# Optimization experiments

Measured on AMD Instinct MI355X. Metric: run time of the kernel, lower is better.

Reference implementation:

```python
import jax, jax.numpy as jnp
import numpy as np

B, N, M, C1, C2, H = 16, 4096, 1024, 256, 512, 256
SE_C = max(1, int(H / 24.0))  # 10
BN_EPS = 1e-5

def _bn(x, g, b):
    # training-mode BatchNorm over (B, n) per channel; x: [B, C, n]
    mean = jnp.mean(x, axis=(0, 2), keepdims=True)
    var = jnp.mean((x - mean) ** 2, axis=(0, 2), keepdims=True)  # biased var (torch)
    return (x - mean) * jax.lax.rsqrt(var + BN_EPS) * g[None, :, None] + b[None, :, None]

def _swish(x):
    return x * jax.nn.sigmoid(x)

def setup_inputs() -> dict:
    key = jax.random.key(0)
    ks = jax.random.split(key, 12)
    d = {
        "unknown": jax.random.normal(ks[0], (B, N, 3), jnp.float32),
        "known": jax.random.normal(ks[1], (B, M, 3), jnp.float32),
        "unknow_feats": jax.random.normal(ks[2], (B, C1, N), jnp.float32),
        "known_feats": jax.random.normal(ks[3], (B, C2, M), jnp.float32),
        # conv1 (C1+C2 -> H), no bias (bn)
        "W1": jax.random.normal(ks[4], (H, C1 + C2), jnp.float32) * (1.0 / np.sqrt(C1 + C2)),
        "g1": jnp.ones((H,), jnp.float32),
        "b1": jnp.zeros((H,), jnp.float32),
        # SE block (1x1 convs with bias, no pooling in this impl)
        "se_rw": jax.random.normal(ks[5], (SE_C, H), jnp.float32) * (1.0 / np.sqrt(H)),
        "se_rb": jnp.zeros((SE_C,), jnp.float32),
        "se_ew": jax.random.normal(ks[6], (H, SE_C), jnp.float32) * (1.0 / np.sqrt(SE_C)),
        "se_eb": jnp.zeros((H,), jnp.float32),
        # conv2 (H -> H), no bias
        "W2": jax.random.normal(ks[7], (H, H), jnp.float32) * (1.0 / np.sqrt(H)),
        "g2": jnp.ones((H,), jnp.float32),
        "b2": jnp.zeros((H,), jnp.float32),
    }
    return d

def reference(unknown, known, unknow_feats, known_feats,
              W1, g1, b1, se_rw, se_rb, se_ew, se_eb, W2, g2, b2):
    # three_nn: squared distances of each unknown point to all known points
    d2 = jnp.sum((unknown[:, :, None, :] - known[:, None, :, :]) ** 2, axis=-1)  # [B,N,M]
    neg_d, idx = jax.lax.top_k(-d2, 3)  # 3 smallest
    dist = -neg_d                                       # [B,N,3]
    dist_recip = 1.0 / (dist + 1e-8)
    weight = dist_recip / jnp.sum(dist_recip, axis=2, keepdims=True)  # [B,N,3]
    # three_interpolate: gather known_feats at idx, inverse-distance weighted sum
    gathered = jnp.take_along_axis(known_feats[:, :, None, :], idx[:, None, :, :], axis=3)  # [B,C2,N,3]
    interp = jnp.sum(gathered * weight[:, None, :, :], axis=-1)  # [B,C2,N]
    x = jnp.concatenate([interp, unknow_feats], axis=1)  # [B,C1+C2,N]
    # conv1 (1x1) + BN + SE
    h = jnp.einsum('oc,bcn->bon', W1, x)
    h = _bn(h, g1, b1)
    s = jnp.einsum('oc,bcn->bon', se_rw, h) + se_rb[None, :, None]
    s = _swish(s)
    s = jnp.einsum('oc,bcn->bon', se_ew, s) + se_eb[None, :, None]
    h = jax.nn.sigmoid(s) * h
    # conv2 (1x1) + BN + ReLU
    h = jnp.einsum('oc,bcn->bon', W2, h)
    h = _bn(h, g2, b2)
    return jax.nn.relu(h)  # [B, H, N]
```

## Files before the change

kernel.cpp:

```cpp
#include <hip/hip_runtime.h>
#include <math.h>

#define B_ 16
#define N_ 4096
#define M_ 1024
#define C1_ 256
#define C2_ 512
#define H_ 256
#define SEC_ 10
#define PARTS_ 128
#define BN_EPS 1e-5f

typedef _Float16 f16;
typedef f16 f16x8 __attribute__((ext_vector_type(8)));
typedef f16 f16x4 __attribute__((ext_vector_type(4)));
typedef f16 f16x2 __attribute__((ext_vector_type(2)));
typedef float f32x4 __attribute__((ext_vector_type(4)));

__global__ __launch_bounds__(256)
void three_nn_kernel(const float* __restrict__ unknown, const float* __restrict__ known,
                     int* __restrict__ idxp, float* __restrict__ wgtp)
{
    __shared__ float kx[M_], ky[M_], kz[M_];
    __shared__ float cd[4][64][3];
    __shared__ int   ci[4][64][3];
    const int b  = blockIdx.y;
    const int bn = blockIdx.x * 64;
    const int t  = threadIdx.x;
    const float* kb = known + (long)b * M_ * 3;

    {
        const float4 q0 = *(const float4*)(kb + 12*t);
        const float4 q1 = *(const float4*)(kb + 12*t + 4);
        const float4 q2 = *(const float4*)(kb + 12*t + 8);
        const int m = 4*t;
        kx[m+0]=q0.x; ky[m+0]=q0.y; kz[m+0]=q0.z;
        kx[m+1]=q0.w; ky[m+1]=q1.x; kz[m+1]=q1.y;
        kx[m+2]=q1.z; ky[m+2]=q1.w; kz[m+2]=q2.x;
        kx[m+3]=q2.y; ky[m+3]=q2.z; kz[m+3]=q2.w;
    }
    __syncthreads();

    const int w = t >> 6, ln = t & 63;
    const int n = bn + ln;
    const float* up = unknown + ((long)b * N_ + n) * 3;
    const float ux = up[0], uy = up[1], uz = up[2];

    float b0 = 1e30f, b1v = 1e30f, b2v = 1e30f;
    int j0 = 0, j1 = 0, j2 = 0;

    const int m0 = w * 256;
    for (int m = m0; m < m0 + 256; m += 4) {
        const float4 X = *(const float4*)&kx[m];
        const float4 Y = *(const float4*)&ky[m];
        const float4 Z = *(const float4*)&kz[m];
        const float px[4] = {X.x, X.y, X.z, X.w};
        const float py[4] = {Y.x, Y.y, Y.z, Y.w};
        const float pz[4] = {Z.x, Z.y, Z.z, Z.w};
        #pragma unroll
        for (int q = 0; q < 4; q++) {
            const float dx = ux - px[q], dy = uy - py[q], dz = uz - pz[q];
            const float d = dx*dx + dy*dy + dz*dz;
            if (d < b2v) {
                const int mm = m + q;
                if (d < b1v) {
                    b2v = b1v; j2 = j1;
                    if (d < b0) { b1v = b0; j1 = j0; b0 = d; j0 = mm; }
                    else        { b1v = d;  j1 = mm; }
                } else { b2v = d; j2 = mm; }
            }
        }
    }
    cd[w][ln][0] = b0;  cd[w][ln][1] = b1v; cd[w][ln][2] = b2v;
    ci[w][ln][0] = j0;  ci[w][ln][1] = j1;  ci[w][ln][2] = j2;
    __syncthreads();

    if (t < 64) {
        float d0 = cd[0][t][0], d1 = cd[0][t][1], d2 = cd[0][t][2];
        int   i0 = ci[0][t][0], i1 = ci[0][t][1], i2 = ci[0][t][2];
        #pragma unroll
        for (int c = 1; c < 4; c++) {
            #pragma unroll
            for (int j = 0; j < 3; j++) {
                const float d = cd[c][t][j];
                const int  ix = ci[c][t][j];
                if (d < d2) {
                    if (d < d1) {
                        d2 = d1; i2 = i1;
                        if (d < d0) { d1 = d0; i1 = i0; d0 = d; i0 = ix; }
                        else        { d1 = d;  i1 = ix; }
                    } else { d2 = d; i2 = ix; }
                }
            }
        }
        const float r0 = 1.f/(d0 + 1e-8f), r1 = 1.f/(d1 + 1e-8f), r2 = 1.f/(d2 + 1e-8f);
        const float rs = 1.f/(r0 + r1 + r2);
        const long base = ((long)b * N_ + bn + t) * 3;
        idxp[base+0] = i0; idxp[base+1] = i1; idxp[base+2] = i2;
        wgtp[base+0] = r0*rs; wgtp[base+1] = r1*rs; wgtp[base+2] = r2*rs;
    }
}

__global__ __launch_bounds__(256)
void convert_w_kernel(const float* __restrict__ W1, const float* __restrict__ W2,
                      f16* __restrict__ Wf0, f16* __restrict__ Wf1, f16* __restrict__ Wf2)
{
    const int which = blockIdx.y;
    const int K8    = (which == 0) ? 64 : 32;
    const int lda   = (which == 2) ? 256 : 768;
    const float* src = (which == 0) ? W1 : (which == 1) ? (W1 + 512) : W2;
    f16* dst = (which == 0) ? Wf0 : (which == 1) ? Wf1 : Wf2;
    const int t = blockIdx.x * 256 + threadIdx.x;
    const int total = 16 * K8 * 16;
    if (t >= total) return;
    const int l16 = t & 15;
    const int fi  = t >> 4;
    const int k8  = fi & (K8 - 1);
    const int rb  = fi >> ((which == 0) ? 6 : 5);
    const float* s = src + (long)(rb*16 + l16)*lda + k8*8;
    const float4 a = *(const float4*)s;
    const float4 c = *(const float4*)(s + 4);
    f16x8 h;
    h[0]=(f16)a.x; h[1]=(f16)a.y; h[2]=(f16)a.z; h[3]=(f16)a.w;
    h[4]=(f16)c.x; h[5]=(f16)c.y; h[6]=(f16)c.z; h[7]=(f16)c.w;
    *(f16x8*)&dst[(long)t*8] = h;
}

template<int MODE>
__global__ __launch_bounds__(256)
void gemm_mfma(const f16* __restrict__ Af, int K,
               const float* __restrict__ Bf, const f16* __restrict__ Bh,
               long strideB, int ldb,
               f16* __restrict__ Ch, long strideC, int ldc,
               const f16* __restrict__ Gt,
               const int* __restrict__ idxp, const float* __restrict__ wgtp,
               float* __restrict__ psum,
               const float* __restrict__ ssum, const float* __restrict__ rbAdj,
               const float* __restrict__ se_ewp, const float* __restrict__ se_ebp,
               const float* __restrict__ a1p, const float* __restrict__ c1p)
{
    constexpr int TILE = 32 * 72;
    __shared__ __align__(16) f16 smem[32*264];
    __shared__ float sswl[SEC_*32];
    f16* const BsA = smem;
    f16* const BsB = smem + TILE;

    const int b   = blockIdx.z;
    const int bn  = blockIdx.x * 32;
    const int tid = threadIdx.x;
    const int l = tid & 63, w = tid >> 6;
    const int lane16 = l & 15, quad = l >> 4;
    const int K8 = K >> 3;

    const float* Bfb = nullptr;
    const f16*   Bhb = nullptr;
    if constexpr (MODE == 2) Bhb = Bh + (long)b*strideB;
    else                     Bfb = Bf + (long)b*strideB;

    if constexpr (MODE == 2) {
        for (int i = tid; i < SEC_*32; i += 256) {
            const int j = i >> 5, nn = i & 31;
            const float v = rbAdj[j] + ssum[((long)b*SEC_ + j)*N_ + bn + nn];
            sswl[j*32 + nn] = v / (1.f + __expf(-v));
        }
        __syncthreads();
    }

    f32x4 acc[4][2];
    #pragma unroll
    for (int i = 0; i < 4; i++)
        #pragma unroll
        for (int j = 0; j < 2; j++)
            acc[i][j] = (f32x4){0.f, 0.f, 0.f, 0.f};

    const int k2a = tid >> 3;
    const int n0a = (tid & 7) * 4;
    auto stageB = [&](int k0, f16* __restrict__ Bsb) {
        if constexpr (MODE == 2) {
            const int ka = k0 + 2*k2a;
            const f16* s0 = Bhb + (long)ka*ldb + bn + n0a;
            const f16x4 ua = *(const f16x4*)s0;
            const f16x4 ub = *(const f16x4*)(s0 + ldb);
            float val[2][4];
            #pragma unroll
            for (int r = 0; r < 2; r++) {
                const int kr = ka + r;
                const float aa = a1p[kr], cc = c1p[kr], eb = se_ebp[kr];
                const float* ew = se_ewp + kr*SEC_;
                #pragma unroll
                for (int j = 0; j < 4; j++) {
                    float e = eb;
                    #pragma unroll
                    for (int q = 0; q < SEC_; q++) e += ew[q]*sswl[q*32 + n0a + j];
                    const float g  = 1.f/(1.f + __expf(-e));
                    const float hv = (r == 0) ? (float)ua[j] : (float)ub[j];
                    val[r][j] = g * (aa*hv + cc);
                }
            }
            #pragma unroll
            for (int j = 0; j < 4; j++) {
                f16x2 p; p[0] = (f16)val[0][j]; p[1] = (f16)val[1][j];
                *(f16x2*)&Bsb[(n0a+j)*72 + 2*k2a] = p;
            }
        } else {
            const float* s0 = Bfb + (long)(k0 + 2*k2a)*ldb + bn + n0a;
            const float4 u = *(const float4*)s0;
            const float4 v = *(const float4*)(s0 + ldb);
            f16x2 p0, p1, p2, p3;
            p0[0]=(f16)u.x; p0[1]=(f16)v.x;
            p1[0]=(f16)u.y; p1[1]=(f16)v.y;
            p2[0]=(f16)u.z; p2[1]=(f16)v.z;
            p3[0]=(f16)u.w; p3[1]=(f16)v.w;
            *(f16x2*)&Bsb[(n0a+0)*72 + 2*k2a] = p0;
            *(f16x2*)&Bsb[(n0a+1)*72 + 2*k2a] = p1;
            *(f16x2*)&Bsb[(n0a+2)*72 + 2*k2a] = p2;
            *(f16x2*)&Bsb[(n0a+3)*72 + 2*k2a] = p3;
        }
    };

    const f16* Afp = Af + quad*128 + lane16*8;
    const int bbase = lane16*72 + quad*8;

    stageB(0, BsA);
    __syncthreads();

    const int NKT = K >> 6;
    int cur = 0;
    for (int kt = 0; kt < NKT; kt++) {
        f16* const Bcur = cur ? BsB : BsA;
        if (kt + 1 < NKT) stageB((kt+1) << 6, cur ? BsA : BsB);
        #pragma unroll
        for (int s = 0; s < 2; s++) {
            const int ks = kt*2 + s;
            f16x8 af[4], bf[2];
            #pragma unroll
            for (int i = 0; i < 4; i++)
                af[i] = *(const f16x8*)(Afp + (long)((w*4 + i)*K8 + ks*4)*128);
            #pragma unroll
            for (int j = 0; j < 2; j++)
                bf[j] = *(const f16x8*)&Bcur[bbase + j*1152 + s*32];
            #pragma unroll
            for (int i = 0; i < 4; i++)
                #pragma unroll
                for (int j = 0; j < 2; j++)
                    acc[i][j] = __builtin_amdgcn_mfma_f32_16x16x32_f16(af[i], bf[j], acc[i][j], 0, 0, 0);
        }
        __syncthreads();
        cur ^= 1;
    }

    if constexpr (MODE == 0) {
        f16* Gl = smem;
        #pragma unroll
        for (int i = 0; i < 4; i++)
            #pragma unroll
            for (int r = 0; r < 4; r++) {
                const int h = w*64 + i*16 + quad*4 + r;
                #pragma unroll
                for (int j = 0; j < 2; j++)
                    Gl[(j*16 + lane16)*264 + h] = (f16)acc[i][j][r];
            }
        __syncthreads();
        f16* Gtb = Ch + (long)b*strideC + (long)bn*H_;
        #pragma unroll
        for (int it = 0; it < 4; it++) {
            const int t = it*256 + tid;
            const int m = t >> 5, c = (t & 31)*8;
            *(f16x8*)&Gtb[m*H_ + c] = *(const f16x8*)&Gl[m*264 + c];
        }
    } else {
        if constexpr (MODE == 1) {
            f16* P = smem;
            const int p  = tid >> 3;
            const int qd = tid & 7;
            const long ib = ((long)b*N_ + bn + p)*3;
            const int i0 = idxp[ib], i1 = idxp[ib+1], i2 = idxp[ib+2];
            const float w0 = wgtp[ib], w1 = wgtp[ib+1], w2 = wgtp[ib+2];
            const f16* gb = Gt + (long)b*M_*H_;
            const f16* g0 = gb + (long)i0*H_ + qd*32;
            const f16* g1 = gb + (long)i1*H_ + qd*32;
            const f16* g2 = gb + (long)i2*H_ + qd*32;
            f16* Pr = P + p*264 + qd*32;
            #pragma unroll
            for (int c = 0; c < 32; c += 8) {
                const f16x8 x0 = *(const f16x8*)&g0[c];
                const f16x8 x1 = *(const f16x8*)&g1[c];
                const f16x8 x2 = *(const f16x8*)&g2[c];
                f16x8 o;
                #pragma unroll
                for (int e = 0; e < 8; e++)
                    o[e] = (f16)(w0*(float)x0[e] + w1*(float)x1[e] + w2*(float)x2[e]);
                *(f16x8*)&Pr[c] = o;
            }
            __syncthreads();
            #pragma unroll
            for (int i = 0; i < 4; i++)
                #pragma unroll
                for (int r = 0; r < 4; r++) {
                    const int h = w*64 + i*16 + quad*4 + r;
                    #pragma unroll
                    for (int j = 0; j < 2; j++)
                        acc[i][j][r] += (float)P[(j*16 + lane16)*264 + h];
                }
        }
        const int bid = blockIdx.z * gridDim.x + blockIdx.x;
        float* ps = psum + (long)bid * (2*H_);
        f16* Cb = Ch + (long)b*strideC;
        #pragma unroll
        for (int i = 0; i < 4; i++)
            #pragma unroll
            for (int r = 0; r < 4; r++) {
                const int row = w*64 + i*16 + quad*4 + r;
                float s1 = 0.f, s2 = 0.f;
                #pragma unroll
                for (int j = 0; j < 2; j++) {
                    const float v = acc[i][j][r];
                    s1 += v; s2 += v*v;
                    Cb[(long)row*ldc + bn + j*16 + lane16] = (f16)v;
                }
                #pragma unroll
                for (int off = 1; off < 16; off <<= 1) {
                    s1 += __shfl_xor(s1, off, 64);
                    s2 += __shfl_xor(s2, off, 64);
                }
                if (lane16 == 0) {
                    ps[row]      = s1;
                    ps[H_ + row] = s2;
                }
            }
    }
}

__global__ __launch_bounds__(256)
void reduce_stats1_kernel(const float* __restrict__ psum, float* __restrict__ partial,
                          int nblk)
{
    const int chunk = nblk / PARTS_;
    const int r0 = blockIdx.x * chunk;
    const int t  = threadIdx.x;
    float a0 = 0.f, a1 = 0.f;
    #pragma unroll 4
    for (int r = r0; r < r0 + chunk; r++) {
        a0 += psum[(long)r*(2*H_) + t];
        a1 += psum[(long)r*(2*H_) + t + H_];
    }
    partial[(long)blockIdx.x*(2*H_) + t]      = a0;
    partial[(long)blockIdx.x*(2*H_) + t + H_] = a1;
}

__global__ __launch_bounds__(256)
void finalize1_kernel(const float* __restrict__ partial,
                      const float* __restrict__ g, const float* __restrict__ bb,
                      const float* __restrict__ se_rw, const float* __restrict__ se_rb,
                      float* __restrict__ a1, float* __restrict__ c1,
                      float* __restrict__ rw2, float* __restrict__ rbAdj)
{
    __shared__ float cbuf[H_];
    __shared__ float red[256];
    const int o = threadIdx.x;
    float S1 = 0.f, S2 = 0.f;
    #pragma unroll 4
    for (int r = 0; r < PARTS_; r++) {
        S1 += partial[(long)r*(2*H_) + o];
        S2 += partial[(long)r*(2*H_) + o + H_];
    }
    const float inv = 1.f / (float)(B_ * N_);
    const float mean = S1 * inv;
    const float var  = S2 * inv - mean*mean;
    const float a = g[o] * rsqrtf(var + BN_EPS);
    const float c = bb[o] - mean*a;
    a1[o] = a; c1[o] = c; cbuf[o] = c;
    for (int j = 0; j < SEC_; j++) rw2[j*H_ + o] = se_rw[j*H_ + o] * a;
    __syncthreads();
    for (int j = 0; j < SEC_; j++) {
        red[o] = se_rw[j*H_ + o] * cbuf[o];
        __syncthreads();
        for (int s = 128; s > 0; s >>= 1) {
            if (o < s) red[o] += red[o + s];
            __syncthreads();
        }
        if (o == 0) rbAdj[j] = se_rb[j] + red[0];
        __syncthreads();
    }
}

__global__ __launch_bounds__(256)
void se_reduce_kernel(const f16* __restrict__ h1h, const float* __restrict__ rw2,
                      float* __restrict__ ssum)
{
    __shared__ float rwl[SEC_][H_];
    const int b = blockIdx.y;
    const int n = blockIdx.x*256 + threadIdx.x;
    for (int i = threadIdx.x; i < SEC_*H_; i += 256)
        rwl[i >> 8][i & 255] = rw2[i];
    __syncthreads();
    float acc[SEC_];
    #pragma unroll
    for (int j = 0; j < SEC_; j++) acc[j] = 0.f;
    const f16* hp = h1h + (long)b*H_*N_ + n;
    #pragma unroll 8
    for (int o = 0; o < H_; o++) {
        const float hv = (float)hp[(long)o*N_];
        #pragma unroll
        for (int j = 0; j < SEC_; j++) acc[j] += rwl[j][o]*hv;
    }
    #pragma unroll
    for (int j = 0; j < SEC_; j++)
        ssum[((long)b*SEC_ + j)*N_ + n] = acc[j];
}

__global__ __launch_bounds__(256)
void finalize2_kernel(const float* __restrict__ partial,
                      const float* __restrict__ g, const float* __restrict__ bb,
                      float* __restrict__ a2, float* __restrict__ c2)
{
    const int o = threadIdx.x;
    float S1 = 0.f, S2 = 0.f;
    #pragma unroll 4
    for (int r = 0; r < PARTS_; r++) {
        S1 += partial[(long)r*(2*H_) + o];
        S2 += partial[(long)r*(2*H_) + o + H_];
    }
    const float inv = 1.f / (float)(B_ * N_);
    const float mean = S1 * inv;
    const float var  = S2 * inv - mean*mean;
    const float a = g[o] * rsqrtf(var + BN_EPS);
    a2[o] = a; c2[o] = bb[o] - mean*a;
}

__global__ __launch_bounds__(256)
void bn_relu_kernel(const f16* __restrict__ h2h, float* __restrict__ out,
                    const float* __restrict__ a2, const float* __restrict__ c2)
{
    const long e = ((long)blockIdx.x*256 + threadIdx.x)*8;
    const int o = (int)((e >> 12) & (H_ - 1));
    const f16x8 v = *(const f16x8*)(h2h + e);
    const float a = a2[o], c = c2[o];
    float4 r0, r1;
    r0.x = fmaxf(a*(float)v[0] + c, 0.f);
    r0.y = fmaxf(a*(float)v[1] + c, 0.f);
    r0.z = fmaxf(a*(float)v[2] + c, 0.f);
    r0.w = fmaxf(a*(float)v[3] + c, 0.f);
    r1.x = fmaxf(a*(float)v[4] + c, 0.f);
    r1.y = fmaxf(a*(float)v[5] + c, 0.f);
    r1.z = fmaxf(a*(float)v[6] + c, 0.f);
    r1.w = fmaxf(a*(float)v[7] + c, 0.f);
    *(float4*)(out + e)     = r0;
    *(float4*)(out + e + 4) = r1;
}

extern "C" void kernel_launch(void* const* d_in, const int* in_sizes, int n_in,
                              void* d_out, int out_size, void* d_ws, size_t ws_size,
                              hipStream_t stream)
{
    const float* unknown = (const float*)d_in[0];
    const float* known   = (const float*)d_in[1];
    const float* uf      = (const float*)d_in[2];
    const float* kf      = (const float*)d_in[3];
    const float* W1      = (const float*)d_in[4];
    const float* g1      = (const float*)d_in[5];
    const float* b1      = (const float*)d_in[6];
    const float* se_rw   = (const float*)d_in[7];
    const float* se_rb   = (const float*)d_in[8];
    const float* se_ew   = (const float*)d_in[9];
    const float* se_eb   = (const float*)d_in[10];
    const float* W2      = (const float*)d_in[11];
    const float* g2      = (const float*)d_in[12];
    const float* b2      = (const float*)d_in[13];

    char* ws = (char*)d_ws;
    size_t off = 0;
    auto alloc = [&](size_t bytes) -> void* {
        void* p = ws + off;
        off += (bytes + 255) & ~(size_t)255;
        return p;
    };
    const int NBLK = (N_/32) * B_;
    int*   idxp   = (int*)  alloc((size_t)B_*N_*3*4);
    float* wgtp   = (float*)alloc((size_t)B_*N_*3*4);
    f16*   Gt     = (f16*)  alloc((size_t)B_*M_*H_*2);
    f16*   h1h    = (f16*)  alloc((size_t)B_*H_*N_*2);
    f16*   h2h    = (f16*)  alloc((size_t)B_*H_*N_*2);
    float* ssum   = (float*)alloc((size_t)B_*SEC_*N_*4);
    float* psum1  = (float*)alloc((size_t)NBLK*2*H_*4);
    float* psum2  = (float*)alloc((size_t)NBLK*2*H_*4);
    float* part1  = (float*)alloc((size_t)PARTS_*2*H_*4);
    float* part2  = (float*)alloc((size_t)PARTS_*2*H_*4);
    float* a1     = (float*)alloc(H_*4);
    float* c1     = (float*)alloc(H_*4);
    float* rw2    = (float*)alloc(SEC_*H_*4);
    float* rbAdj  = (float*)alloc(64*4);
    float* a2     = (float*)alloc(H_*4);
    float* c2     = (float*)alloc(H_*4);
    f16*   Wf0    = (f16*)  alloc((size_t)H_*C2_*2);
    f16*   Wf1    = (f16*)  alloc((size_t)H_*C1_*2);
    f16*   Wf2    = (f16*)  alloc((size_t)H_*H_*2);
    (void)ws_size; (void)in_sizes; (void)n_in; (void)out_size;

    float* out = (float*)d_out;

    convert_w_kernel<<<dim3(64, 3), 256, 0, stream>>>(W1, W2, Wf0, Wf1, Wf2);

    three_nn_kernel<<<dim3(N_/64, B_), 256, 0, stream>>>(unknown, known, idxp, wgtp);

    gemm_mfma<0><<<dim3(M_/32, 1, B_), 256, 0, stream>>>(
        Wf0, C2_, kf, nullptr, (long)C2_*M_, M_,
        Gt, (long)M_*H_, 0,
        nullptr, nullptr, nullptr, nullptr,
        nullptr, nullptr, nullptr, nullptr, nullptr, nullptr);

    gemm_mfma<1><<<dim3(N_/32, 1, B_), 256, 0, stream>>>(
        Wf1, C1_, uf, nullptr, (long)C1_*N_, N_,
        h1h, (long)H_*N_, N_,
        Gt, idxp, wgtp, psum1,
        nullptr, nullptr, nullptr, nullptr, nullptr, nullptr);

    reduce_stats1_kernel<<<dim3(PARTS_), 256, 0, stream>>>(psum1, part1, NBLK);

    finalize1_kernel<<<1, 256, 0, stream>>>(part1, g1, b1, se_rw, se_rb, a1, c1, rw2, rbAdj);

    se_reduce_kernel<<<dim3(N_/256, B_), 256, 0, stream>>>(h1h, rw2, ssum);

    gemm_mfma<2><<<dim3(N_/32, 1, B_), 256, 0, stream>>>(
        Wf2, H_, nullptr, h1h, (long)H_*N_, N_,
        h2h, (long)H_*N_, N_,
        nullptr, nullptr, nullptr, psum2,
        ssum, rbAdj, se_ew, se_eb, a1, c1);

    reduce_stats1_kernel<<<dim3(PARTS_), 256, 0, stream>>>(psum2, part2, NBLK);

    finalize2_kernel<<<1, 256, 0, stream>>>(part2, g2, b2, a2, c2);

    bn_relu_kernel<<<dim3((unsigned)((long)B_*H_*N_/2048)), 256, 0, stream>>>(h2h, out, a2, c2);
}
```

Before: 362.0 us.

## Fuse SE reduce into conv2 GEMM via shared-memory staged h1 tile

Removes the separate se_reduce kernel and its ssum buffer. Each conv2 GEMM block now loads its full 256x32 h1 tile into shared memory once, computes the SE squeeze dot products there, and reuses the staged tile during B-operand staging instead of rereading global memory. This saves a kernel launch and the round trip of ssum plus a second read of h1. In exchange it uses more LDS per block, which may lower occupancy, and adds a serial 256-long dot product per thread (320 outputs over 256 threads) before the GEMM starts.

```diff
diff --git a/kernel.cpp b/kernel.cpp
--- a/kernel.cpp
+++ b/kernel.cpp
@@ -135,15 +135,18 @@
                const f16* __restrict__ Gt,
                const int* __restrict__ idxp, const float* __restrict__ wgtp,
                float* __restrict__ psum,
-               const float* __restrict__ ssum, const float* __restrict__ rbAdj,
+               const float* __restrict__ aux, const float* __restrict__ rbAdj,
                const float* __restrict__ se_ewp, const float* __restrict__ se_ebp,
                const float* __restrict__ a1p, const float* __restrict__ c1p)
 {
     constexpr int TILE = 32 * 72;
-    __shared__ __align__(16) f16 smem[32*264];
+    constexpr int RAWS = 32 * 266;
+    constexpr int SMEMH = (MODE == 2) ? (2*TILE + RAWS) : (32*264);
+    __shared__ __align__(16) f16 smem[SMEMH];
     __shared__ float sswl[SEC_*32];
     f16* const BsA = smem;
     f16* const BsB = smem + TILE;
+    f16* const raw = (MODE == 2) ? (smem + 2*TILE) : nullptr;
 
     const int b   = blockIdx.z;
     const int bn  = blockIdx.x * 32;
@@ -157,11 +160,35 @@
     if constexpr (MODE == 2) Bhb = Bh + (long)b*strideB;
     else                     Bfb = Bf + (long)b*strideB;
 
+    const int k2a = tid >> 3;
+    const int n0a = (tid & 7) * 4;
+
     if constexpr (MODE == 2) {
+        f16x4 ra[4][2];
+        #pragma unroll
+        for (int kt = 0; kt < 4; kt++) {
+            const f16* s0 = Bhb + (long)(kt*64 + 2*k2a)*ldb + bn + n0a;
+            ra[kt][0] = *(const f16x4*)s0;
+            ra[kt][1] = *(const f16x4*)(s0 + ldb);
+        }
+        #pragma unroll
+        for (int kt = 0; kt < 4; kt++) {
+            const int ka = kt*64 + 2*k2a;
+            #pragma unroll
+            for (int j = 0; j < 4; j++) {
+                f16x2 p; p[0] = ra[kt][0][j]; p[1] = ra[kt][1][j];
+                *(f16x2*)&raw[(n0a+j)*266 + ka] = p;
+            }
+        }
+        __syncthreads();
         for (int i = tid; i < SEC_*32; i += 256) {
             const int j = i >> 5, nn = i & 31;
-            const float v = rbAdj[j] + ssum[((long)b*SEC_ + j)*N_ + bn + nn];
-            sswl[j*32 + nn] = v / (1.f + __expf(-v));
+            float acc = rbAdj[j];
+            const float* rwj = aux + j*H_;
+            const f16* rr = raw + nn*266;
+            #pragma unroll 8
+            for (int o = 0; o < H_; o++) acc += rwj[o] * (float)rr[o];
+            sswl[j*32 + nn] = acc / (1.f + __expf(-acc));
         }
         __syncthreads();
     }
@@ -173,14 +200,9 @@
         for (int j = 0; j < 2; j++)
             acc[i][j] = (f32x4){0.f, 0.f, 0.f, 0.f};
 
-    const int k2a = tid >> 3;
-    const int n0a = (tid & 7) * 4;
     auto stageB = [&](int k0, f16* __restrict__ Bsb) {
         if constexpr (MODE == 2) {
             const int ka = k0 + 2*k2a;
-            const f16* s0 = Bhb + (long)ka*ldb + bn + n0a;
-            const f16x4 ua = *(const f16x4*)s0;
-            const f16x4 ub = *(const f16x4*)(s0 + ldb);
             float val[2][4];
             #pragma unroll
             for (int r = 0; r < 2; r++) {
@@ -193,7 +215,7 @@
                     #pragma unroll
                     for (int q = 0; q < SEC_; q++) e += ew[q]*sswl[q*32 + n0a + j];
                     const float g  = 1.f/(1.f + __expf(-e));
-                    const float hv = (r == 0) ? (float)ua[j] : (float)ub[j];
+                    const float hv = (float)raw[(n0a+j)*266 + kr];
                     val[r][j] = g * (aa*hv + cc);
                 }
             }
@@ -382,31 +404,6 @@
         if (o == 0) rbAdj[j] = se_rb[j] + red[0];
         __syncthreads();
     }
-}
-
-__global__ __launch_bounds__(256)
-void se_reduce_kernel(const f16* __restrict__ h1h, const float* __restrict__ rw2,
-                      float* __restrict__ ssum)
-{
-    __shared__ float rwl[SEC_][H_];
-    const int b = blockIdx.y;
-    const int n = blockIdx.x*256 + threadIdx.x;
-    for (int i = threadIdx.x; i < SEC_*H_; i += 256)
-        rwl[i >> 8][i & 255] = rw2[i];
-    __syncthreads();
-    float acc[SEC_];
-    #pragma unroll
-    for (int j = 0; j < SEC_; j++) acc[j] = 0.f;
-    const f16* hp = h1h + (long)b*H_*N_ + n;
-    #pragma unroll 8
-    for (int o = 0; o < H_; o++) {
-        const float hv = (float)hp[(long)o*N_];
-        #pragma unroll
-        for (int j = 0; j < SEC_; j++) acc[j] += rwl[j][o]*hv;
-    }
-    #pragma unroll
-    for (int j = 0; j < SEC_; j++)
-        ssum[((long)b*SEC_ + j)*N_ + n] = acc[j];
 }
 
 __global__ __launch_bounds__(256)
@@ -481,7 +478,6 @@
     f16*   Gt     = (f16*)  alloc((size_t)B_*M_*H_*2);
     f16*   h1h    = (f16*)  alloc((size_t)B_*H_*N_*2);
     f16*   h2h    = (f16*)  alloc((size_t)B_*H_*N_*2);
-    float* ssum   = (float*)alloc((size_t)B_*SEC_*N_*4);
     float* psum1  = (float*)alloc((size_t)NBLK*2*H_*4);
     float* psum2  = (float*)alloc((size_t)NBLK*2*H_*4);
     float* part1  = (float*)alloc((size_t)PARTS_*2*H_*4);
@@ -519,13 +515,11 @@
 
     finalize1_kernel<<<1, 256, 0, stream>>>(part1, g1, b1, se_rw, se_rb, a1, c1, rw2, rbAdj);
 
-    se_reduce_kernel<<<dim3(N_/256, B_), 256, 0, stream>>>(h1h, rw2, ssum);
-
     gemm_mfma<2><<<dim3(N_/32, 1, B_), 256, 0, stream>>>(
         Wf2, H_, nullptr, h1h, (long)H_*N_, N_,
         h2h, (long)H_*N_, N_,
         nullptr, nullptr, nullptr, psum2,
-        ssum, rbAdj, se_ew, se_eb, a1, c1);
+        rw2, rbAdj, se_ew, se_eb, a1, c1);
 
     reduce_stats1_kernel<<<dim3(PARTS_), 256, 0, stream>>>(psum2, part2, NBLK);
 
```

Result: slower. 376.8 us (+4.1%).
